# Optimization experiments

Hardware: AMD Instinct MI355X
Metric: run time of the kernel (lower is better)

Reference implementation:

```python
import jax, jax.numpy as jnp
import numpy as np

N = 50000      # nodes
E = 800000     # edges (avg degree 16)
D = 128        # hidden_channels
FFN = 512
BOT = 64
L = 3          # number of stacked GCN layers


def setup_inputs() -> dict:
    key = jax.random.key(0)
    ks = jax.random.split(key, 10)
    x = jax.random.normal(ks[0], (N, D), dtype=jnp.float32)
    edge_index = jax.random.randint(ks[1], (2, E), 0, N, dtype=jnp.int64)
    s = np.float32(1.0 / np.sqrt(D))
    conv_W = jax.random.normal(ks[2], (L, D, D), dtype=jnp.float32) * s
    conv_b = jnp.zeros((L, D), dtype=jnp.float32)
    fc1_w = jax.random.normal(ks[3], (D, FFN), dtype=jnp.float32) * s
    fc1_b = jnp.zeros((FFN,), dtype=jnp.float32)
    fc2_w = jax.random.normal(ks[4], (FFN, BOT), dtype=jnp.float32) * np.float32(1.0 / np.sqrt(FFN))
    fc2_b = jnp.zeros((BOT,), dtype=jnp.float32)
    return {"x": x, "edge_index": edge_index, "conv_W": conv_W, "conv_b": conv_b,
            "fc1_w": fc1_w, "fc1_b": fc1_b, "fc2_w": fc2_w, "fc2_b": fc2_b}


def _gcn_conv(x, src, dst, W, b):
    """GCNConv: D^{-1/2} (A+I) D^{-1/2} X W + b, degree computed with self-loops."""
    n = x.shape[0]
    deg = jax.ops.segment_sum(jnp.ones(src.shape[0], x.dtype), dst, num_segments=n) + 1.0
    norm = jax.lax.rsqrt(deg)                      # [N]
    xw = x @ W                                     # [N, D] transform before scatter
    coef = (norm[src] * norm[dst])[:, None]        # [E, 1]
    agg = jax.ops.segment_sum(xw[src] * coef, dst, num_segments=n)  # gather-scale-scatter
    return agg + xw * (norm * norm)[:, None] + b   # self-loop term + bias


def reference(x, edge_index, conv_W, conv_b, fc1_w, fc1_b, fc2_w, fc2_b):
    src, dst = edge_index[0], edge_index[1]
    for l in range(L):
        x = jax.nn.relu(_gcn_conv(x, src, dst, conv_W[l], conv_b[l]))
        # dropout = identity in eval mode
    x = jax.nn.relu(x @ fc1_w + fc1_b)
    return x @ fc2_w + fc2_b
```

## Files before the change

### kernel.cpp

```cpp
#include <hip/hip_runtime.h>
#include <hip/hip_fp16.h>

#define D 128
#define FFN 512
#define BOT 64
#define EPB 4096

typedef _Float16 f16x8 __attribute__((ext_vector_type(8)));
typedef float f32x4 __attribute__((ext_vector_type(4)));


__global__ __launch_bounds__(256) void k_bcnt(const int* __restrict__ dst, int* __restrict__ bcnt, int nE) {
  __shared__ int h[256];
  int t = threadIdx.x;
  h[t] = 0;
  __syncthreads();
  int base = blockIdx.x * EPB;
  #pragma unroll
  for (int m = 0; m < EPB / 256; ++m) {
    int idx = base + m * 256 + t;
    if (idx < nE) atomicAdd(&h[dst[idx] >> 8], 1);
  }
  __syncthreads();
  if (h[t] > 0) atomicAdd(&bcnt[t], h[t]);
}

__global__ __launch_bounds__(256) void k_bscan(const int* __restrict__ bcnt, int* __restrict__ boff,
                                               int* __restrict__ bcur, int nbkt, int nE) {
  __shared__ int s[256];
  int t = threadIdx.x;
  int v = (t < nbkt) ? bcnt[t] : 0;
  s[t] = v;
  __syncthreads();
  for (int d = 1; d < 256; d <<= 1) {
    int add = (t >= d) ? s[t - d] : 0;
    __syncthreads();
    s[t] += add;
    __syncthreads();
  }
  int ex = s[t] - v;
  boff[t] = ex;
  bcur[t] = ex;
  if (t == 255) boff[256] = nE;
  if (t >= nbkt) boff[t] = nE;
}

__global__ __launch_bounds__(256) void k_bscatter(const int* __restrict__ ei, int* __restrict__ bcur,
                                                  uint2* __restrict__ bed, int nE) {
  __shared__ uint2 st[EPB];
  __shared__ int cnt[256], off[256], base[256], cur[256];
  int t = threadIdx.x;
  int blk0 = blockIdx.x * EPB;
  int nblk = nE - blk0;
  if (nblk > EPB) nblk = EPB;

  cnt[t] = 0;
  cur[t] = 0;
  __syncthreads();

  int rs[EPB / 256], rd[EPB / 256];
  #pragma unroll
  for (int m = 0; m < EPB / 256; ++m) {
    int idx = blk0 + m * 256 + t;
    if (idx < nE) {
      rs[m] = ei[idx];
      rd[m] = ei[nE + idx];
      atomicAdd(&cnt[rd[m] >> 8], 1);
    } else {
      rd[m] = -1;
    }
  }
  __syncthreads();

  int v = cnt[t];
  off[t] = v;
  __syncthreads();
  for (int d = 1; d < 256; d <<= 1) {
    int add = (t >= d) ? off[t - d] : 0;
    __syncthreads();
    off[t] += add;
    __syncthreads();
  }
  int ex = off[t] - v;
  __syncthreads();
  off[t] = ex;
  base[t] = (v > 0) ? atomicAdd(&bcur[t], v) : 0;
  __syncthreads();

  #pragma unroll
  for (int m = 0; m < EPB / 256; ++m) {
    if (rd[m] >= 0) {
      int b = rd[m] >> 8;
      int p = off[b] + atomicAdd(&cur[b], 1);
      st[p] = make_uint2((unsigned)rs[m], (unsigned)rd[m]);
    }
  }
  __syncthreads();

  for (int j = t; j < nblk; j += 256) {
    uint2 pr = st[j];
    int b = (int)(pr.y >> 8);
    bed[base[b] + (j - off[b])] = pr;
  }
}

__global__ __launch_bounds__(256) void k_bcsr(const uint2* __restrict__ bed, const int* __restrict__ boff,
                                              int* __restrict__ rowptr, float* __restrict__ nrm,
                                              int* __restrict__ col, int N, int nE) {
  __shared__ int cnt[256], noff[256], cur[256];
  int t = threadIdx.x;
  int b = blockIdx.x;
  int e0 = boff[b], e1 = boff[b + 1];

  cnt[t] = 0;
  __syncthreads();
  for (int j = e0 + t; j < e1; j += 256)
    atomicAdd(&cnt[bed[j].y & 255], 1);
  __syncthreads();

  int v = cnt[t];
  noff[t] = v;
  __syncthreads();
  for (int d = 1; d < 256; d <<= 1) {
    int add = (t >= d) ? noff[t - d] : 0;
    __syncthreads();
    noff[t] += add;
    __syncthreads();
  }
  int ex = noff[t] - v;
  __syncthreads();
  noff[t] = ex;
  cur[t] = ex;
  __syncthreads();

  int node = (b << 8) + t;
  if (node < N) {
    rowptr[node] = e0 + ex;
    nrm[node] = rsqrtf((float)v + 1.0f);
  }
  if (b == 0 && t == 0) rowptr[N] = nE;

  for (int j = e0 + t; j < e1; j += 256) {
    uint2 pr = bed[j];
    int d2 = (int)(pr.y & 255);
    int p = atomicAdd(&cur[d2], 1);
    col[e0 + p] = (int)pr.x;
  }
}


__global__ __launch_bounds__(256) void k_split(const float* __restrict__ X,
                                               __half* __restrict__ Xh, __half* __restrict__ Xl, int n8) {
  int i = blockIdx.x * 256 + threadIdx.x;
  if (i >= n8) return;
  float4 a = ((const float4*)X)[i * 2];
  float4 b = ((const float4*)X)[i * 2 + 1];
  float v[8] = {a.x, a.y, a.z, a.w, b.x, b.y, b.z, b.w};
  __half2 hh[4], ll[4];
  #pragma unroll
  for (int q = 0; q < 4; ++q) {
    __half h0 = __float2half_rn(v[2 * q]);
    __half h1 = __float2half_rn(v[2 * q + 1]);
    __half l0 = __float2half_rn(v[2 * q] - __half2float(h0));
    __half l1 = __float2half_rn(v[2 * q + 1] - __half2float(h1));
    hh[q] = __halves2half2(h0, h1);
    ll[q] = __halves2half2(l0, l1);
  }
  *(uint4*)(Xh + (size_t)i * 8) = *(uint4*)hh;
  *(uint4*)(Xl + (size_t)i * 8) = *(uint4*)ll;
}

__global__ __launch_bounds__(256) void k_splitw(const float* __restrict__ W,
                                                __half* __restrict__ WhT, __half* __restrict__ WlT,
                                                int K, int N) {
  int id = blockIdx.x * 256 + threadIdx.x;
  if (id >= K * N) return;
  int n = id / K, k = id % K;
  float v = W[(size_t)k * N + n];
  __half h = __float2half_rn(v);
  WhT[id] = h;
  WlT[id] = __float2half_rn(v - __half2float(h));
}

__global__ __launch_bounds__(256) void k_splitwc(const float* __restrict__ W,
                                                 __half* __restrict__ WhT, __half* __restrict__ WlT,
                                                 int total) {
  int id = blockIdx.x * 256 + threadIdx.x;
  if (id >= total) return;
  int l = id / (D * D), r = id % (D * D);
  int n = r / D, k = r % D;
  float v = W[(size_t)l * D * D + (size_t)k * D + n];
  __half h = __float2half_rn(v);
  WhT[id] = h;
  WlT[id] = __float2half_rn(v - __half2float(h));
}


__global__ __launch_bounds__(256, 4)
void k_conv(const __half* __restrict__ Ah_g, const __half* __restrict__ Al_g,
            const __half* __restrict__ BhT_g, const __half* __restrict__ BlT_g,
            const float* __restrict__ aux, __half* __restrict__ Yo, int M) {
  __shared__ __half Ahs[64][40];
  __shared__ __half Als[64][40];
  __shared__ __half Bhs[128][40];
  __shared__ __half Bls[128][40];

  const int t = threadIdx.x;
  const int rbase = blockIdx.x * 64;
  const int lane = t & 63, wid = t >> 6;
  const int wr = (wid >> 1) * 32;
  const int wc = (wid & 1) * 64;
  const int lr = lane & 15, lq = lane >> 4;

  f32x4 acc[2][4];
  #pragma unroll
  for (int m = 0; m < 2; ++m)
    #pragma unroll
    for (int n = 0; n < 4; ++n) acc[m][n] = (f32x4){0.f, 0.f, 0.f, 0.f};

  for (int kc = 0; kc < D; kc += 32) {
    __syncthreads();
    {
      int row = t >> 2, q = t & 3;
      int gr = rbase + row;
      uint4 vh = {0, 0, 0, 0}, vl = {0, 0, 0, 0};
      if (gr < M) {
        vh = *(const uint4*)(Ah_g + (size_t)gr * D + kc + q * 8);
        vl = *(const uint4*)(Al_g + (size_t)gr * D + kc + q * 8);
      }
      *(uint4*)&Ahs[row][q * 8] = vh;
      *(uint4*)&Als[row][q * 8] = vl;
    }
    #pragma unroll
    for (int mm = 0; mm < 2; ++mm) {
      int idx = mm * 256 + t;
      int c = idx >> 2, q = idx & 3;
      size_t src = (size_t)c * D + kc + q * 8;
      *(uint4*)&Bhs[c][q * 8] = *(const uint4*)(BhT_g + src);
      *(uint4*)&Bls[c][q * 8] = *(const uint4*)(BlT_g + src);
    }
    __syncthreads();

    f16x8 fa[2], fal[2], fb[4], fbl[4];
    #pragma unroll
    for (int m = 0; m < 2; ++m) {
      fa[m]  = *(const f16x8*)&Ahs[wr + m * 16 + lr][lq * 8];
      fal[m] = *(const f16x8*)&Als[wr + m * 16 + lr][lq * 8];
    }
    #pragma unroll
    for (int n = 0; n < 4; ++n) {
      fb[n]  = *(const f16x8*)&Bhs[wc + n * 16 + lr][lq * 8];
      fbl[n] = *(const f16x8*)&Bls[wc + n * 16 + lr][lq * 8];
    }
    #pragma unroll
    for (int m = 0; m < 2; ++m)
      #pragma unroll
      for (int n = 0; n < 4; ++n) {
        acc[m][n] = __builtin_amdgcn_mfma_f32_16x16x32_f16(fa[m], fb[n], acc[m][n], 0, 0, 0);
        acc[m][n] = __builtin_amdgcn_mfma_f32_16x16x32_f16(fa[m], fbl[n], acc[m][n], 0, 0, 0);
        acc[m][n] = __builtin_amdgcn_mfma_f32_16x16x32_f16(fal[m], fb[n], acc[m][n], 0, 0, 0);
      }
  }

  #pragma unroll
  for (int m = 0; m < 2; ++m)
    #pragma unroll
    for (int j = 0; j < 4; ++j) {
      int row = rbase + wr + m * 16 + lq * 4 + j;
      if (row < M) {
        float s = aux[row];
        #pragma unroll
        for (int n = 0; n < 4; ++n) {
          int colg = wc + n * 16 + lr;
          Yo[(size_t)row * D + colg] = __float2half_rn(acc[m][n][j] * s);
        }
      }
    }
}


__global__ __launch_bounds__(256, 2)
void k_mlp(const __half* __restrict__ Xh_g, const __half* __restrict__ Xl_g,
           const __half* __restrict__ W1hT, const __half* __restrict__ W1lT,
           const float* __restrict__ B1,
           const __half* __restrict__ W2hT, const __half* __restrict__ W2lT,
           const float* __restrict__ B2,
           float* __restrict__ Out, int M) {
  __shared__ __half Xhs[64][136], Xls[64][136];
  __shared__ __half Ws[2][64][136];
  __shared__ __half Hs[64][72];

  const int t = threadIdx.x;
  const int rbase = blockIdx.x * 64;
  const int lane = t & 63, wid = t >> 6;
  const int wr = (wid >> 1) * 32;
  const int wcn = (wid & 1) * 32;
  const int lr = lane & 15, lq = lane >> 4;

  #pragma unroll
  for (int mm = 0; mm < 4; ++mm) {
    int idx = mm * 256 + t;
    int row = idx >> 4, q = idx & 15;
    int gr = rbase + row;
    uint4 vh = {0, 0, 0, 0}, vl = {0, 0, 0, 0};
    if (gr < M) {
      vh = *(const uint4*)(Xh_g + (size_t)gr * D + q * 8);
      vl = *(const uint4*)(Xl_g + (size_t)gr * D + q * 8);
    }
    *(uint4*)&Xhs[row][q * 8] = vh;
    *(uint4*)&Xls[row][q * 8] = vl;
  }

  f32x4 accO[2][2];
  #pragma unroll
  for (int m = 0; m < 2; ++m)
    #pragma unroll
    for (int n = 0; n < 2; ++n) accO[m][n] = (f32x4){0.f, 0.f, 0.f, 0.f};

  for (int ch = 0; ch < FFN / 64; ++ch) {
    __syncthreads();
    #pragma unroll
    for (int mm = 0; mm < 4; ++mm) {
      int idx = mm * 256 + t;
      int c = idx >> 4, q = idx & 15;
      size_t src = (size_t)(ch * 64 + c) * D + q * 8;
      *(uint4*)&Ws[0][c][q * 8] = *(const uint4*)(W1hT + src);
      *(uint4*)&Ws[1][c][q * 8] = *(const uint4*)(W1lT + src);
    }
    __syncthreads();

    f32x4 accH[2][2];
    #pragma unroll
    for (int m = 0; m < 2; ++m)
      #pragma unroll
      for (int n = 0; n < 2; ++n) accH[m][n] = (f32x4){0.f, 0.f, 0.f, 0.f};

    #pragma unroll
    for (int kf = 0; kf < 4; ++kf) {
      f16x8 fa[2], fal[2], fb[2], fbl[2];
      #pragma unroll
      for (int m = 0; m < 2; ++m) {
        fa[m]  = *(const f16x8*)&Xhs[wr + m * 16 + lr][kf * 32 + lq * 8];
        fal[m] = *(const f16x8*)&Xls[wr + m * 16 + lr][kf * 32 + lq * 8];
      }
      #pragma unroll
      for (int n = 0; n < 2; ++n) {
        fb[n]  = *(const f16x8*)&Ws[0][wcn + n * 16 + lr][kf * 32 + lq * 8];
        fbl[n] = *(const f16x8*)&Ws[1][wcn + n * 16 + lr][kf * 32 + lq * 8];
      }
      #pragma unroll
      for (int m = 0; m < 2; ++m)
        #pragma unroll
        for (int n = 0; n < 2; ++n) {
          accH[m][n] = __builtin_amdgcn_mfma_f32_16x16x32_f16(fa[m], fb[n], accH[m][n], 0, 0, 0);
          accH[m][n] = __builtin_amdgcn_mfma_f32_16x16x32_f16(fa[m], fbl[n], accH[m][n], 0, 0, 0);
          accH[m][n] = __builtin_amdgcn_mfma_f32_16x16x32_f16(fal[m], fb[n], accH[m][n], 0, 0, 0);
        }
    }

    {
      float bb1[2];
      #pragma unroll
      for (int n = 0; n < 2; ++n) bb1[n] = B1[ch * 64 + wcn + n * 16 + lr];
      #pragma unroll
      for (int m = 0; m < 2; ++m)
        #pragma unroll
        for (int n = 0; n < 2; ++n)
          #pragma unroll
          for (int j = 0; j < 4; ++j) {
            int rl = wr + m * 16 + lq * 4 + j;
            int cl = wcn + n * 16 + lr;
            Hs[rl][cl] = __float2half_rn(fmaxf(accH[m][n][j] + bb1[n], 0.f));
          }
    }
    __syncthreads();
    #pragma unroll
    for (int mm = 0; mm < 2; ++mm) {
      int idx = mm * 256 + t;
      int c = idx >> 3, q = idx & 7;
      size_t src = (size_t)c * FFN + ch * 64 + q * 8;
      *(uint4*)&Ws[0][c][q * 8] = *(const uint4*)(W2hT + src);
      *(uint4*)&Ws[1][c][q * 8] = *(const uint4*)(W2lT + src);
    }
    __syncthreads();

    #pragma unroll
    for (int s = 0; s < 2; ++s) {
      f16x8 fha[2], fwb[2], fwbl[2];
      #pragma unroll
      for (int m = 0; m < 2; ++m)
        fha[m] = *(const f16x8*)&Hs[wr + m * 16 + lr][s * 32 + lq * 8];
      #pragma unroll
      for (int n = 0; n < 2; ++n) {
        fwb[n]  = *(const f16x8*)&Ws[0][wcn + n * 16 + lr][s * 32 + lq * 8];
        fwbl[n] = *(const f16x8*)&Ws[1][wcn + n * 16 + lr][s * 32 + lq * 8];
      }
      #pragma unroll
      for (int m = 0; m < 2; ++m)
        #pragma unroll
        for (int n = 0; n < 2; ++n) {
          accO[m][n] = __builtin_amdgcn_mfma_f32_16x16x32_f16(fha[m], fwb[n], accO[m][n], 0, 0, 0);
          accO[m][n] = __builtin_amdgcn_mfma_f32_16x16x32_f16(fha[m], fwbl[n], accO[m][n], 0, 0, 0);
        }
    }
  }

  #pragma unroll
  for (int m = 0; m < 2; ++m)
    #pragma unroll
    for (int j = 0; j < 4; ++j) {
      int row = rbase + wr + m * 16 + lq * 4 + j;
      if (row < M) {
        #pragma unroll
        for (int n = 0; n < 2; ++n) {
          int colg = wcn + n * 16 + lr;
          Out[(size_t)row * BOT + colg] = accO[m][n][j] + B2[colg];
        }
      }
    }
}


__global__ __launch_bounds__(256) void k_agg(const __half* __restrict__ Y,
                                             const int* __restrict__ rowptr, const int* __restrict__ col,
                                             const float* __restrict__ nrm, const float* __restrict__ bias,
                                             __half* __restrict__ Xh, __half* __restrict__ Xl, int n) {
  int gtid = blockIdx.x * 256 + threadIdx.x;
  int node = gtid >> 4;
  int sl = threadIdx.x & 15;
  if (node >= n) return;
  const uint4* Yv = (const uint4*)Y;

  float s0[8] = {0.f, 0.f, 0.f, 0.f, 0.f, 0.f, 0.f, 0.f};
  float s1[8] = {0.f, 0.f, 0.f, 0.f, 0.f, 0.f, 0.f, 0.f};
  auto up = [](uint4 v, float* a) {
    __half2* hp = (__half2*)&v;
    #pragma unroll
    for (int q = 0; q < 4; ++q) {
      float2 f = __half22float2(hp[q]);
      a[2 * q] += f.x;
      a[2 * q + 1] += f.y;
    }
  };
  up(Yv[(size_t)node * 16 + sl], s0);
  int e0 = rowptr[node], e1 = rowptr[node + 1];
  int e = e0;
  for (; e + 4 <= e1; e += 4) {
    int c0 = col[e], c1 = col[e + 1], c2 = col[e + 2], c3 = col[e + 3];
    uint4 v0 = Yv[(size_t)c0 * 16 + sl];
    uint4 v1 = Yv[(size_t)c1 * 16 + sl];
    uint4 v2 = Yv[(size_t)c2 * 16 + sl];
    uint4 v3 = Yv[(size_t)c3 * 16 + sl];
    up(v0, s0); up(v1, s1); up(v2, s0); up(v3, s1);
  }
  for (; e < e1; ++e) up(Yv[(size_t)col[e] * 16 + sl], s0);

  float nm = nrm[node];
  const float* bp = bias + sl * 8;
  __half h[8], l[8];
  #pragma unroll
  for (int q = 0; q < 8; ++q) {
    float o = fmaxf(fmaf(s0[q] + s1[q], nm, bp[q]), 0.f);
    h[q] = __float2half_rn(o);
    l[q] = __float2half_rn(o - __half2float(h[q]));
  }
  ((uint4*)Xh)[(size_t)node * 16 + sl] = *(uint4*)h;
  ((uint4*)Xl)[(size_t)node * 16 + sl] = *(uint4*)l;
}

extern "C" void kernel_launch(void* const* d_in, const int* in_sizes, int n_in,
                              void* d_out, int out_size, void* d_ws, size_t ws_size,
                              hipStream_t stream) {
  const float* x     = (const float*)d_in[0];
  const int*   ei    = (const int*)d_in[1];
  const float* convW = (const float*)d_in[2];
  const float* convB = (const float*)d_in[3];
  const float* w1    = (const float*)d_in[4];
  const float* b1    = (const float*)d_in[5];
  const float* w2    = (const float*)d_in[6];
  const float* b2    = (const float*)d_in[7];
  float* out = (float*)d_out;

  int N = in_sizes[0] / D;
  int E = in_sizes[1] / 2;
  int L = in_sizes[2] / (D * D);
  int NBKT = (N + 255) >> 8;

  char* ws = (char*)d_ws;
  size_t off = 0;
  auto alloc = [&](size_t bytes) -> char* {
    char* p = ws + off;
    off += (bytes + 255) & ~(size_t)255;
    return p;
  };
  float*  nrm    = (float*)alloc((size_t)N * 4);
  int*    rowptr = (int*)alloc((size_t)(N + 1) * 4);
  int*    col    = (int*)alloc((size_t)E * 4);
  int*    bcnt   = (int*)alloc(512 * 4);
  int*    boff   = (int*)alloc(512 * 4);
  int*    bcur   = (int*)alloc(512 * 4);
  uint2*  bed    = (uint2*)alloc((size_t)E * 8);
  __half* Xh     = (__half*)alloc((size_t)N * D * 2);
  __half* Xl     = (__half*)alloc((size_t)N * D * 2);
  __half* Yh     = (__half*)alloc((size_t)N * D * 2);
  __half* WcTh   = (__half*)alloc((size_t)L * D * D * 2);
  __half* WcTl   = (__half*)alloc((size_t)L * D * D * 2);
  __half* W1Th   = (__half*)alloc((size_t)D * FFN * 2);
  __half* W1Tl   = (__half*)alloc((size_t)D * FFN * 2);
  __half* W2Th   = (__half*)alloc((size_t)FFN * BOT * 2);
  __half* W2Tl   = (__half*)alloc((size_t)FFN * BOT * 2);

  int gS = (E + EPB - 1) / EPB;
  hipMemsetAsync(bcnt, 0, 512 * 4, stream);
  k_bcnt<<<gS, 256, 0, stream>>>(ei + E, bcnt, E);
  k_bscan<<<1, 256, 0, stream>>>(bcnt, boff, bcur, NBKT, E);
  k_bscatter<<<gS, 256, 0, stream>>>(ei, bcur, bed, E);
  k_bcsr<<<NBKT, 256, 0, stream>>>(bed, boff, rowptr, nrm, col, N, E);

  int n8 = N * D / 8;
  k_split<<<(n8 + 255) / 256, 256, 0, stream>>>(x, Xh, Xl, n8);
  k_splitwc<<<(L * D * D + 255) / 256, 256, 0, stream>>>(convW, WcTh, WcTl, L * D * D);
  k_splitw<<<(D * FFN + 255) / 256, 256, 0, stream>>>(w1, W1Th, W1Tl, D, FFN);
  k_splitw<<<(FFN * BOT + 255) / 256, 256, 0, stream>>>(w2, W2Th, W2Tl, FFN, BOT);

  int nRB = (N + 63) / 64;
  for (int l = 0; l < L; ++l) {
    k_conv<<<nRB, 256, 0, stream>>>(
        Xh, Xl, WcTh + (size_t)l * D * D, WcTl + (size_t)l * D * D, nrm, Yh, N);
    k_agg<<<(N * 16 + 255) / 256, 256, 0, stream>>>(Yh, rowptr, col, nrm, convB + (size_t)l * D,
                                                    Xh, Xl, N);
  }

  k_mlp<<<nRB, 256, 0, stream>>>(Xh, Xl, W1Th, W1Tl, b1, W2Th, W2Tl, b2, out, N);
}
```

Before: 252.4 us.

## Hold activation fragments in registers and prefetch MLP weights into registers

k_conv now loads the full 128x128 hi/lo weight matrices into LDS once and reads the activation A fragments straight from global memory into registers. This removes the per-k-chunk double sync and the LDS staging of A, at the cost of more LDS per block, so launch bounds drop to 2 blocks per SM. k_mlp also keeps the X fragments in registers instead of LDS and software-prefetches the next W1 chunk into registers while the current chunk computes. The sync points are rearranged to match, which raises register pressure.

```diff
diff --git a/kernel.cpp b/kernel.cpp
--- a/kernel.cpp
+++ b/kernel.cpp
@@ -196,14 +196,11 @@
 }
 
 
-__global__ __launch_bounds__(256, 4)
-void k_conv(const __half* __restrict__ Ah_g, const __half* __restrict__ Al_g,
-            const __half* __restrict__ BhT_g, const __half* __restrict__ BlT_g,
+__global__ __launch_bounds__(256, 2)
+void k_conv(const __half* __restrict__ Xh_g, const __half* __restrict__ Xl_g,
+            const __half* __restrict__ WhT, const __half* __restrict__ WlT,
             const float* __restrict__ aux, __half* __restrict__ Yo, int M) {
-  __shared__ __half Ahs[64][40];
-  __shared__ __half Als[64][40];
-  __shared__ __half Bhs[128][40];
-  __shared__ __half Bls[128][40];
+  __shared__ __half Bhs[128][136], Bls[128][136];
 
   const int t = threadIdx.x;
   const int rbase = blockIdx.x * 64;
@@ -212,53 +209,54 @@
   const int wc = (wid & 1) * 64;
   const int lr = lane & 15, lq = lane >> 4;
 
+  #pragma unroll
+  for (int mm = 0; mm < 8; ++mm) {
+    int idx = mm * 256 + t;
+    int c = idx >> 4, q = idx & 15;
+    size_t src = (size_t)c * D + q * 8;
+    *(uint4*)&Bhs[c][q * 8] = *(const uint4*)(WhT + src);
+    *(uint4*)&Bls[c][q * 8] = *(const uint4*)(WlT + src);
+  }
+
+  f16x8 fa[2][4], fal[2][4];
+  #pragma unroll
+  for (int m = 0; m < 2; ++m) {
+    int row = rbase + wr + m * 16 + lr;
+    bool ok = row < M;
+    #pragma unroll
+    for (int kf = 0; kf < 4; ++kf) {
+      uint4 vh = {0, 0, 0, 0}, vl = {0, 0, 0, 0};
+      if (ok) {
+        vh = *(const uint4*)(Xh_g + (size_t)row * D + kf * 32 + lq * 8);
+        vl = *(const uint4*)(Xl_g + (size_t)row * D + kf * 32 + lq * 8);
+      }
+      fa[m][kf] = *(f16x8*)&vh;
+      fal[m][kf] = *(f16x8*)&vl;
+    }
+  }
+  __syncthreads();
+
   f32x4 acc[2][4];
   #pragma unroll
   for (int m = 0; m < 2; ++m)
     #pragma unroll
     for (int n = 0; n < 4; ++n) acc[m][n] = (f32x4){0.f, 0.f, 0.f, 0.f};
 
-  for (int kc = 0; kc < D; kc += 32) {
-    __syncthreads();
-    {
-      int row = t >> 2, q = t & 3;
-      int gr = rbase + row;
-      uint4 vh = {0, 0, 0, 0}, vl = {0, 0, 0, 0};
-      if (gr < M) {
-        vh = *(const uint4*)(Ah_g + (size_t)gr * D + kc + q * 8);
-        vl = *(const uint4*)(Al_g + (size_t)gr * D + kc + q * 8);
-      }
-      *(uint4*)&Ahs[row][q * 8] = vh;
-      *(uint4*)&Als[row][q * 8] = vl;
-    }
-    #pragma unroll
-    for (int mm = 0; mm < 2; ++mm) {
-      int idx = mm * 256 + t;
-      int c = idx >> 2, q = idx & 3;
-      size_t src = (size_t)c * D + kc + q * 8;
-      *(uint4*)&Bhs[c][q * 8] = *(const uint4*)(BhT_g + src);
-      *(uint4*)&Bls[c][q * 8] = *(const uint4*)(BlT_g + src);
-    }
-    __syncthreads();
-
-    f16x8 fa[2], fal[2], fb[4], fbl[4];
-    #pragma unroll
-    for (int m = 0; m < 2; ++m) {
-      fa[m]  = *(const f16x8*)&Ahs[wr + m * 16 + lr][lq * 8];
-      fal[m] = *(const f16x8*)&Als[wr + m * 16 + lr][lq * 8];
-    }
+  #pragma unroll
+  for (int kf = 0; kf < 4; ++kf) {
+    f16x8 fb[4], fbl[4];
     #pragma unroll
     for (int n = 0; n < 4; ++n) {
-      fb[n]  = *(const f16x8*)&Bhs[wc + n * 16 + lr][lq * 8];
-      fbl[n] = *(const f16x8*)&Bls[wc + n * 16 + lr][lq * 8];
+      fb[n]  = *(const f16x8*)&Bhs[wc + n * 16 + lr][kf * 32 + lq * 8];
+      fbl[n] = *(const f16x8*)&Bls[wc + n * 16 + lr][kf * 32 + lq * 8];
     }
     #pragma unroll
     for (int m = 0; m < 2; ++m)
       #pragma unroll
       for (int n = 0; n < 4; ++n) {
-        acc[m][n] = __builtin_amdgcn_mfma_f32_16x16x32_f16(fa[m], fb[n], acc[m][n], 0, 0, 0);
-        acc[m][n] = __builtin_amdgcn_mfma_f32_16x16x32_f16(fa[m], fbl[n], acc[m][n], 0, 0, 0);
-        acc[m][n] = __builtin_amdgcn_mfma_f32_16x16x32_f16(fal[m], fb[n], acc[m][n], 0, 0, 0);
+        acc[m][n] = __builtin_amdgcn_mfma_f32_16x16x32_f16(fa[m][kf], fb[n], acc[m][n], 0, 0, 0);
+        acc[m][n] = __builtin_amdgcn_mfma_f32_16x16x32_f16(fa[m][kf], fbl[n], acc[m][n], 0, 0, 0);
+        acc[m][n] = __builtin_amdgcn_mfma_f32_16x16x32_f16(fal[m][kf], fb[n], acc[m][n], 0, 0, 0);
       }
   }
 
@@ -286,9 +284,8 @@
            const __half* __restrict__ W2hT, const __half* __restrict__ W2lT,
            const float* __restrict__ B2,
            float* __restrict__ Out, int M) {
-  __shared__ __half Xhs[64][136], Xls[64][136];
   __shared__ __half Ws[2][64][136];
-  __shared__ __half Hs[64][72];
+  __shared__ __half Hs[64][80];
 
   const int t = threadIdx.x;
   const int rbase = blockIdx.x * 64;
@@ -297,18 +294,30 @@
   const int wcn = (wid & 1) * 32;
   const int lr = lane & 15, lq = lane >> 4;
 
-  #pragma unroll
-  for (int mm = 0; mm < 4; ++mm) {
-    int idx = mm * 256 + t;
-    int row = idx >> 4, q = idx & 15;
-    int gr = rbase + row;
-    uint4 vh = {0, 0, 0, 0}, vl = {0, 0, 0, 0};
-    if (gr < M) {
-      vh = *(const uint4*)(Xh_g + (size_t)gr * D + q * 8);
-      vl = *(const uint4*)(Xl_g + (size_t)gr * D + q * 8);
-    }
-    *(uint4*)&Xhs[row][q * 8] = vh;
-    *(uint4*)&Xls[row][q * 8] = vl;
+  f16x8 fa[2][4], fal[2][4];
+  #pragma unroll
+  for (int m = 0; m < 2; ++m) {
+    int row = rbase + wr + m * 16 + lr;
+    bool ok = row < M;
+    #pragma unroll
+    for (int kf = 0; kf < 4; ++kf) {
+      uint4 vh = {0, 0, 0, 0}, vl = {0, 0, 0, 0};
+      if (ok) {
+        vh = *(const uint4*)(Xh_g + (size_t)row * D + kf * 32 + lq * 8);
+        vl = *(const uint4*)(Xl_g + (size_t)row * D + kf * 32 + lq * 8);
+      }
+      fa[m][kf] = *(f16x8*)&vh;
+      fal[m][kf] = *(f16x8*)&vl;
+    }
+  }
+
+  uint4 w1r[8];
+  #pragma unroll
+  for (int mm = 0; mm < 8; ++mm) {
+    int idx = (mm & 3) * 256 + t;
+    int c = idx >> 4, q = idx & 15;
+    const __half* src = (mm < 4 ? W1hT : W1lT) + (size_t)c * D + q * 8;
+    w1r[mm] = *(const uint4*)src;
   }
 
   f32x4 accO[2][2];
@@ -320,14 +329,22 @@
   for (int ch = 0; ch < FFN / 64; ++ch) {
     __syncthreads();
     #pragma unroll
-    for (int mm = 0; mm < 4; ++mm) {
-      int idx = mm * 256 + t;
+    for (int mm = 0; mm < 8; ++mm) {
+      int idx = (mm & 3) * 256 + t;
       int c = idx >> 4, q = idx & 15;
-      size_t src = (size_t)(ch * 64 + c) * D + q * 8;
-      *(uint4*)&Ws[0][c][q * 8] = *(const uint4*)(W1hT + src);
-      *(uint4*)&Ws[1][c][q * 8] = *(const uint4*)(W1lT + src);
-    }
-    __syncthreads();
+      *(uint4*)&Ws[(mm < 4) ? 0 : 1][c][q * 8] = w1r[mm];
+    }
+    __syncthreads();
+
+    if (ch < FFN / 64 - 1) {
+      #pragma unroll
+      for (int mm = 0; mm < 8; ++mm) {
+        int idx = (mm & 3) * 256 + t;
+        int c = idx >> 4, q = idx & 15;
+        const __half* src = (mm < 4 ? W1hT : W1lT) + (size_t)((ch + 1) * 64 + c) * D + q * 8;
+        w1r[mm] = *(const uint4*)src;
+      }
+    }
 
     f32x4 accH[2][2];
     #pragma unroll
@@ -337,12 +354,7 @@
 
     #pragma unroll
     for (int kf = 0; kf < 4; ++kf) {
-      f16x8 fa[2], fal[2], fb[2], fbl[2];
-      #pragma unroll
-      for (int m = 0; m < 2; ++m) {
-        fa[m]  = *(const f16x8*)&Xhs[wr + m * 16 + lr][kf * 32 + lq * 8];
-        fal[m] = *(const f16x8*)&Xls[wr + m * 16 + lr][kf * 32 + lq * 8];
-      }
+      f16x8 fb[2], fbl[2];
       #pragma unroll
       for (int n = 0; n < 2; ++n) {
         fb[n]  = *(const f16x8*)&Ws[0][wcn + n * 16 + lr][kf * 32 + lq * 8];
@@ -352,12 +364,13 @@
       for (int m = 0; m < 2; ++m)
         #pragma unroll
         for (int n = 0; n < 2; ++n) {
-          accH[m][n] = __builtin_amdgcn_mfma_f32_16x16x32_f16(fa[m], fb[n], accH[m][n], 0, 0, 0);
-          accH[m][n] = __builtin_amdgcn_mfma_f32_16x16x32_f16(fa[m], fbl[n], accH[m][n], 0, 0, 0);
-          accH[m][n] = __builtin_amdgcn_mfma_f32_16x16x32_f16(fal[m], fb[n], accH[m][n], 0, 0, 0);
+          accH[m][n] = __builtin_amdgcn_mfma_f32_16x16x32_f16(fa[m][kf], fb[n], accH[m][n], 0, 0, 0);
+          accH[m][n] = __builtin_amdgcn_mfma_f32_16x16x32_f16(fa[m][kf], fbl[n], accH[m][n], 0, 0, 0);
+          accH[m][n] = __builtin_amdgcn_mfma_f32_16x16x32_f16(fal[m][kf], fb[n], accH[m][n], 0, 0, 0);
         }
     }
 
+    __syncthreads();
     {
       float bb1[2];
       #pragma unroll
@@ -373,14 +386,12 @@
             Hs[rl][cl] = __float2half_rn(fmaxf(accH[m][n][j] + bb1[n], 0.f));
           }
     }
-    __syncthreads();
-    #pragma unroll
-    for (int mm = 0; mm < 2; ++mm) {
-      int idx = mm * 256 + t;
+    #pragma unroll
+    for (int mm = 0; mm < 4; ++mm) {
+      int idx = (mm & 1) * 256 + t;
       int c = idx >> 3, q = idx & 7;
-      size_t src = (size_t)c * FFN + ch * 64 + q * 8;
-      *(uint4*)&Ws[0][c][q * 8] = *(const uint4*)(W2hT + src);
-      *(uint4*)&Ws[1][c][q * 8] = *(const uint4*)(W2lT + src);
+      const __half* src = (mm < 2 ? W2hT : W2lT) + (size_t)c * FFN + ch * 64 + q * 8;
+      *(uint4*)&Ws[(mm < 2) ? 0 : 1][c][q * 8] = *(const uint4*)src;
     }
     __syncthreads();
 
```

Result: slower. 314.9 us (+24.8%).

## Stage full weight in LDS once and load A fragments directly to registers

Applied to the files above, without the earlier changes.

The conv GEMM kernel now loads the whole 128x128 split-fp16 weight (hi and lo) into shared memory once, then reads the activation fragments straight from global memory into registers for all four K chunks. This removes the per-K-chunk barrier pairs and the LDS staging of activations. In exchange the shared memory per block grows to about 68KB and register pressure rises, so launch bounds drop to 2 blocks per SM, which lowers occupancy.

```diff
diff --git a/kernel.cpp b/kernel.cpp
--- a/kernel.cpp
+++ b/kernel.cpp
@@ -196,14 +196,11 @@
 }
 
 
-__global__ __launch_bounds__(256, 4)
-void k_conv(const __half* __restrict__ Ah_g, const __half* __restrict__ Al_g,
-            const __half* __restrict__ BhT_g, const __half* __restrict__ BlT_g,
+__global__ __launch_bounds__(256, 2)
+void k_conv(const __half* __restrict__ Xh_g, const __half* __restrict__ Xl_g,
+            const __half* __restrict__ WhT, const __half* __restrict__ WlT,
             const float* __restrict__ aux, __half* __restrict__ Yo, int M) {
-  __shared__ __half Ahs[64][40];
-  __shared__ __half Als[64][40];
-  __shared__ __half Bhs[128][40];
-  __shared__ __half Bls[128][40];
+  __shared__ __half Bhs[128][136], Bls[128][136];
 
   const int t = threadIdx.x;
   const int rbase = blockIdx.x * 64;
@@ -212,53 +209,54 @@
   const int wc = (wid & 1) * 64;
   const int lr = lane & 15, lq = lane >> 4;
 
+  #pragma unroll
+  for (int mm = 0; mm < 8; ++mm) {
+    int idx = mm * 256 + t;
+    int c = idx >> 4, q = idx & 15;
+    size_t src = (size_t)c * D + q * 8;
+    *(uint4*)&Bhs[c][q * 8] = *(const uint4*)(WhT + src);
+    *(uint4*)&Bls[c][q * 8] = *(const uint4*)(WlT + src);
+  }
+
+  f16x8 fa[2][4], fal[2][4];
+  #pragma unroll
+  for (int m = 0; m < 2; ++m) {
+    int row = rbase + wr + m * 16 + lr;
+    bool ok = row < M;
+    #pragma unroll
+    for (int kf = 0; kf < 4; ++kf) {
+      uint4 vh = {0, 0, 0, 0}, vl = {0, 0, 0, 0};
+      if (ok) {
+        vh = *(const uint4*)(Xh_g + (size_t)row * D + kf * 32 + lq * 8);
+        vl = *(const uint4*)(Xl_g + (size_t)row * D + kf * 32 + lq * 8);
+      }
+      fa[m][kf] = *(f16x8*)&vh;
+      fal[m][kf] = *(f16x8*)&vl;
+    }
+  }
+  __syncthreads();
+
   f32x4 acc[2][4];
   #pragma unroll
   for (int m = 0; m < 2; ++m)
     #pragma unroll
     for (int n = 0; n < 4; ++n) acc[m][n] = (f32x4){0.f, 0.f, 0.f, 0.f};
 
-  for (int kc = 0; kc < D; kc += 32) {
-    __syncthreads();
-    {
-      int row = t >> 2, q = t & 3;
-      int gr = rbase + row;
-      uint4 vh = {0, 0, 0, 0}, vl = {0, 0, 0, 0};
-      if (gr < M) {
-        vh = *(const uint4*)(Ah_g + (size_t)gr * D + kc + q * 8);
-        vl = *(const uint4*)(Al_g + (size_t)gr * D + kc + q * 8);
-      }
-      *(uint4*)&Ahs[row][q * 8] = vh;
-      *(uint4*)&Als[row][q * 8] = vl;
-    }
-    #pragma unroll
-    for (int mm = 0; mm < 2; ++mm) {
-      int idx = mm * 256 + t;
-      int c = idx >> 2, q = idx & 3;
-      size_t src = (size_t)c * D + kc + q * 8;
-      *(uint4*)&Bhs[c][q * 8] = *(const uint4*)(BhT_g + src);
-      *(uint4*)&Bls[c][q * 8] = *(const uint4*)(BlT_g + src);
-    }
-    __syncthreads();
-
-    f16x8 fa[2], fal[2], fb[4], fbl[4];
-    #pragma unroll
-    for (int m = 0; m < 2; ++m) {
-      fa[m]  = *(const f16x8*)&Ahs[wr + m * 16 + lr][lq * 8];
-      fal[m] = *(const f16x8*)&Als[wr + m * 16 + lr][lq * 8];
-    }
+  #pragma unroll
+  for (int kf = 0; kf < 4; ++kf) {
+    f16x8 fb[4], fbl[4];
     #pragma unroll
     for (int n = 0; n < 4; ++n) {
-      fb[n]  = *(const f16x8*)&Bhs[wc + n * 16 + lr][lq * 8];
-      fbl[n] = *(const f16x8*)&Bls[wc + n * 16 + lr][lq * 8];
+      fb[n]  = *(const f16x8*)&Bhs[wc + n * 16 + lr][kf * 32 + lq * 8];
+      fbl[n] = *(const f16x8*)&Bls[wc + n * 16 + lr][kf * 32 + lq * 8];
     }
     #pragma unroll
     for (int m = 0; m < 2; ++m)
       #pragma unroll
       for (int n = 0; n < 4; ++n) {
-        acc[m][n] = __builtin_amdgcn_mfma_f32_16x16x32_f16(fa[m], fb[n], acc[m][n], 0, 0, 0);
-        acc[m][n] = __builtin_amdgcn_mfma_f32_16x16x32_f16(fa[m], fbl[n], acc[m][n], 0, 0, 0);
-        acc[m][n] = __builtin_amdgcn_mfma_f32_16x16x32_f16(fal[m], fb[n], acc[m][n], 0, 0, 0);
+        acc[m][n] = __builtin_amdgcn_mfma_f32_16x16x32_f16(fa[m][kf], fb[n], acc[m][n], 0, 0, 0);
+        acc[m][n] = __builtin_amdgcn_mfma_f32_16x16x32_f16(fa[m][kf], fbl[n], acc[m][n], 0, 0, 0);
+        acc[m][n] = __builtin_amdgcn_mfma_f32_16x16x32_f16(fal[m][kf], fb[n], acc[m][n], 0, 0, 0);
       }
   }
 
```

After: 258.4 us. +2.4%, slower.
